# Performance work log

Hardware: AMD Instinct MI355X
Metric: run time of the kernel (lower is better)

## Reference

```python
import jax, jax.numpy as jnp
import numpy as np

B, S, HID = 2, 2048, 2048
H, DH = 16, 128
SCALE = 1.0 / np.sqrt(DH)


def setup_inputs() -> dict:
    key = jax.random.key(0)
    ks = jax.random.split(key, 5)
    std = 1.0 / np.sqrt(HID)
    return {
        "x": jax.random.normal(ks[0], (B, S, HID), dtype=jnp.float32),
        "wq": jax.random.normal(ks[1], (HID, HID), dtype=jnp.float32) * std,
        "wk": jax.random.normal(ks[2], (HID, HID), dtype=jnp.float32) * std,
        "wv": jax.random.normal(ks[3], (HID, HID), dtype=jnp.float32) * std,
        "wo": jax.random.normal(ks[4], (HID, HID), dtype=jnp.float32) * std,
    }


def reference(x, wq, wk, wv, wo):
    # nn.Linear(h, h, bias=False): y = x @ W^T
    q = (x @ wq.T).reshape(B, S, H, DH).transpose(0, 2, 1, 3)  # [B,H,S,Dh]
    k = (x @ wk.T).reshape(B, S, H, DH).transpose(0, 2, 1, 3)
    v = (x @ wv.T).reshape(B, S, H, DH).transpose(0, 2, 1, 3)
    scores = jnp.einsum("bhsd,bhtd->bhst", q, k) * SCALE  # [B,H,S,S]
    attn = jax.nn.softmax(scores.astype(jnp.float32), axis=-1).astype(q.dtype)
    # dropout p=0.0 (eval): identity
    out = jnp.einsum("bhst,bhtd->bhsd", attn, v)  # [B,H,S,Dh]
    out = out.transpose(0, 2, 1, 3).reshape(B, S, HID)
    return out @ wo.T
```

## Files before the change

kernel.cpp:

```cpp
#include <hip/hip_runtime.h>
#include <hip/hip_bf16.h>
#include <stdint.h>

typedef __attribute__((ext_vector_type(8))) short short8;
typedef __attribute__((ext_vector_type(4))) short short4v;
typedef __attribute__((ext_vector_type(4))) float f32x4;
typedef __attribute__((ext_vector_type(4))) unsigned int uint4v;

static __device__ __forceinline__ ushort f2bf(float f) {
    uint32_t u = __builtin_bit_cast(uint32_t, f);
    uint32_t r = (u + 0x7FFFu + ((u >> 16) & 1u)) >> 16;
    return (ushort)r;
}

static __device__ __forceinline__ uint32_t cvt_pk_bf16(float lo, float hi) {
    uint32_t d;
    asm("v_cvt_pk_bf16_f32 %0, %1, %2" : "=v"(d) : "v"(lo), "v"(hi));
    return d;
}

static __device__ __forceinline__ void async_copy16(const void* g, void* l) {
    __builtin_amdgcn_global_load_lds(
        (const __attribute__((address_space(1))) uint32_t*)g,
        (__attribute__((address_space(3))) uint32_t*)l, 16, 0, 0);
}

#define TR16(P3, IMM)                                                        \
    ({                                                                       \
        short4v _d;                                                          \
        asm volatile("ds_read_b64_tr_b16 %0, %1 offset:" #IMM                \
                     : "=v"(_d) : "v"(P3));                                  \
        _d;                                                                  \
    })

#define CAT8(a, b) __builtin_shufflevector(a, b, 0, 1, 2, 3, 4, 5, 6, 7)

__global__ __launch_bounds__(256) void cast_kernel(const float* __restrict__ in,
                                                   ushort* __restrict__ out, int n4) {
    int i = blockIdx.x * 256 + threadIdx.x;
    if (i >= n4) return;
    float4 v = reinterpret_cast<const float4*>(in)[i];
    uint2 o;
    o.x = cvt_pk_bf16(v.x, v.y);
    o.y = cvt_pk_bf16(v.z, v.w);
    reinterpret_cast<uint2*>(out)[i] = o;
}

__global__ __launch_bounds__(256) void cast3_kernel(const float* __restrict__ a,
                                                    const float* __restrict__ b,
                                                    const float* __restrict__ c,
                                                    ushort* __restrict__ out, int n4each) {
    int i = blockIdx.x * 256 + threadIdx.x;
    int which = i / n4each;
    int j = i - which * n4each;
    const float* src = which == 0 ? a : (which == 1 ? b : c);
    if (which > 2) return;
    float4 v = reinterpret_cast<const float4*>(src)[j];
    uint2 o;
    o.x = cvt_pk_bf16(v.x, v.y);
    o.y = cvt_pk_bf16(v.z, v.w);
    reinterpret_cast<uint2*>(out)[i] = o;
}

static __device__ __forceinline__ void store_val(float* C, size_t idx, float v) { C[idx] = v; }
static __device__ __forceinline__ void store_val(ushort* C, size_t idx, float v) { C[idx] = f2bf(v); }

template <typename OutT>
__global__ __launch_bounds__(256) void gemm_bt_kernel(const ushort* __restrict__ A,
                                                      const ushort* __restrict__ B,
                                                      OutT* __restrict__ C,
                                                      int M, int N, int K) {
    __shared__ __align__(16) ushort As[128 * 32];
    __shared__ __align__(16) ushort Bs[128 * 32];
    const int tid = threadIdx.x;
    const int w = tid >> 6, lane = tid & 63;
    const int fr = lane & 15, fq = lane >> 4;
    const int wr = w >> 1, wc = w & 1;
    const int bpn = N >> 7;
    const int which = blockIdx.x / bpn;
    const int row0 = blockIdx.y * 128;
    const int gcol0 = blockIdx.x * 128;
    const int col0 = gcol0 - which * N;
    OutT* Cw = C + (size_t)which * M * N;

    const int srow = tid >> 2;
    const int scol = (tid & 3) * 8;
    const ushort* ga0 = A + (size_t)(row0 + srow) * K + scol;
    const ushort* ga1 = A + (size_t)(row0 + 64 + srow) * K + scol;
    const ushort* gb0 = B + (size_t)(gcol0 + srow) * K + scol;
    const ushort* gb1 = B + (size_t)(gcol0 + 64 + srow) * K + scol;
    ushort* la0 = &As[(w * 64) * 8];
    ushort* la1 = &As[(256 + w * 64) * 8];
    ushort* lb0 = &Bs[(w * 64) * 8];
    ushort* lb1 = &Bs[(256 + w * 64) * 8];

    f32x4 acc[4][4];
#pragma unroll
    for (int m = 0; m < 4; ++m)
#pragma unroll
        for (int n = 0; n < 4; ++n) acc[m][n] = f32x4{0.f, 0.f, 0.f, 0.f};

    for (int kt = 0; kt < K; kt += 32) {
        __syncthreads();
        async_copy16(ga0 + kt, la0);
        async_copy16(ga1 + kt, la1);
        async_copy16(gb0 + kt, lb0);
        async_copy16(gb1 + kt, lb1);
        __syncthreads();
        short8 af[4], bfr[4];
#pragma unroll
        for (int m = 0; m < 4; ++m)
            af[m] = *(const short8*)&As[(wr * 64 + m * 16 + fr) * 32 + fq * 8];
#pragma unroll
        for (int n = 0; n < 4; ++n)
            bfr[n] = *(const short8*)&Bs[(wc * 64 + n * 16 + fr) * 32 + fq * 8];
#pragma unroll
        for (int m = 0; m < 4; ++m)
#pragma unroll
            for (int n = 0; n < 4; ++n)
                acc[m][n] = __builtin_amdgcn_mfma_f32_16x16x32_bf16(af[m], bfr[n], acc[m][n], 0, 0, 0);
    }

#pragma unroll
    for (int m = 0; m < 4; ++m) {
        const int grow = row0 + wr * 64 + m * 16 + fq * 4;
#pragma unroll
        for (int n = 0; n < 4; ++n) {
            const int gcol = col0 + wc * 64 + n * 16 + fr;
#pragma unroll
            for (int r = 0; r < 4; ++r)
                store_val(Cw, (size_t)(grow + r) * N + gcol, acc[m][n][r]);
        }
    }
}

__global__ __launch_bounds__(512, 2) void gemm256_kernel(const ushort* __restrict__ A,
                                                         const ushort* __restrict__ B,
                                                         ushort* __restrict__ C,
                                                         int M, int N, int K) {
    __shared__ __align__(16) char smem[131072];
    const int tid = threadIdx.x, w = tid >> 6, lane = tid & 63;
    const int fr = lane & 15, fq = lane >> 4;
    const int wm = w >> 2, wn = w & 3;
    const int bpn = N >> 8;
    const int which = blockIdx.x / bpn;
    const int row0 = blockIdx.y * 256;
    const int gcol0 = blockIdx.x * 256;
    const int col0 = gcol0 - which * N;
    ushort* Cw = C + (size_t)which * M * N;

    const int lo = ((tid & 7) ^ ((tid >> 3) & 7)) << 4;
    const int r0p = ((tid >> 3) << 1) + (lo >> 6);
    const int colE = (lo & 63) >> 1;
    const ushort* Ap0 = A + (size_t)(row0 + r0p) * K + colE;
    const ushort* Ap1 = A + (size_t)(row0 + 128 + r0p) * K + colE;
    const ushort* Bp0 = B + (size_t)(gcol0 + r0p) * K + colE;
    const ushort* Bp1 = B + (size_t)(gcol0 + 128 + r0p) * K + colE;

    char* aregs = smem;
    char* bregs = smem + 65536;
    const int wbyte = w * 1024;

    auto stageH = [&](int h) {
        const int kc = (h >> 1) * 64 + (h & 1) * 32;
        char* ar = aregs + (h & 3) * 16384;
        char* br = bregs + (h & 3) * 16384;
        async_copy16(Ap0 + kc, ar + wbyte);
        async_copy16(Ap1 + kc, ar + 8192 + wbyte);
        async_copy16(Bp0 + kc, br + wbyte);
        async_copy16(Bp1 + kc, br + 8192 + wbyte);
    };

    const int swz = ((fr & 1) * 64 + fq * 16) ^ (((fr >> 1) & 7) << 4);
    const int aBase = (wm * 64 + (fr >> 1)) * 128 + swz;
    const int bBase = (wn * 32 + (fr >> 1)) * 128 + swz;

    f32x4 acc[8][4];
#pragma unroll
    for (int m = 0; m < 8; ++m)
#pragma unroll
        for (int n = 0; n < 4; ++n) acc[m][n] = f32x4{0.f, 0.f, 0.f, 0.f};

    const int nH = K >> 5;
    stageH(0); stageH(1); stageH(2);
    asm volatile("s_waitcnt vmcnt(8)\n\ts_barrier" ::: "memory");

    for (int i = 0; i < nH; ++i) {
        if (i + 3 < nH) stageH(i + 3);
        const char* ar = aregs + (i & 3) * 16384 + aBase;
        const char* br = bregs + (i & 3) * 16384 + bBase;
        short8 af[8], bf[4];
#pragma unroll
        for (int m = 0; m < 8; ++m) af[m] = *(const short8*)(ar + m * 1024);
#pragma unroll
        for (int n = 0; n < 4; ++n) bf[n] = *(const short8*)(br + n * 1024);
        __builtin_amdgcn_s_setprio(1);
#pragma unroll
        for (int m = 0; m < 8; ++m)
#pragma unroll
            for (int n = 0; n < 4; ++n)
                acc[m][n] = __builtin_amdgcn_mfma_f32_16x16x32_bf16(af[m], bf[n], acc[m][n], 0, 0, 0);
        __builtin_amdgcn_s_setprio(0);
        if (i < nH - 3)
            asm volatile("s_waitcnt vmcnt(8)\n\ts_barrier" ::: "memory");
        else if (i == nH - 3)
            asm volatile("s_waitcnt vmcnt(4)\n\ts_barrier" ::: "memory");
        else if (i == nH - 2)
            asm volatile("s_waitcnt vmcnt(0)\n\ts_barrier" ::: "memory");
    }

#pragma unroll
    for (int m = 0; m < 8; ++m) {
        const int grow = row0 + wm * 128 + m * 16 + fq * 4;
#pragma unroll
        for (int n = 0; n < 4; ++n) {
            const int gcol = col0 + wn * 64 + n * 16 + fr;
#pragma unroll
            for (int r2 = 0; r2 < 4; ++r2)
                Cw[(size_t)(grow + r2) * N + gcol] = f2bf(acc[m][n][r2]);
        }
    }
}

__global__ __launch_bounds__(512) void attn_kernel(const ushort* __restrict__ Q,
                                                   const ushort* __restrict__ K,
                                                   const ushort* __restrict__ V,
                                                   ushort* __restrict__ O,
                                                   int S, int HID, float scale) {
    __shared__ __align__(16) ushort Ks[64 * 128];
    __shared__ __align__(16) ushort Vs[64 * 128];

    const int tid = threadIdx.x, w = tid >> 6, lane = tid & 63;
    const int fr = lane & 15, fq = lane >> 4;
    const int qt = blockIdx.x, h = blockIdx.y, b = blockIdx.z;
    const size_t rs = (size_t)HID;
    const int qr0 = qt * 128 + w * 16;
    const float c1 = scale * 1.4426950408889634f;

    short8 qf[4];
    {
        const ushort* qp = Q + ((size_t)(b * S) + qr0 + fr) * rs + h * 128 + fq * 8;
#pragma unroll
        for (int ks = 0; ks < 4; ++ks) qf[ks] = *(const short8*)(qp + ks * 32);
    }

    f32x4 of[8];
#pragma unroll
    for (int n = 0; n < 8; ++n) of[n] = f32x4{0.f, 0.f, 0.f, 0.f};
    float m2 = -1e30f;
    float l = 0.f;

    const ushort* Kb = K + (size_t)(b * S) * rs + h * 128;
    const ushort* Vb = V + (size_t)(b * S) * rs + h * 128;

    size_t koff[2];
#pragma unroll
    for (int j = 0; j < 2; ++j) {
        int row = j * 32 + w * 4 + (lane >> 4);
        int colb = ((lane & 15) * 16) ^ ((row & 7) << 4);
        koff[j] = (size_t)row * rs + (colb >> 1);
    }
    size_t voff[2];
#pragma unroll
    for (int j = 0; j < 2; ++j) {
        int L = j * 64 + w * 8 + (lane >> 3);
        int kv = (L >> 3) * 4 + ((lane >> 1) & 3);
        int dh = (L & 7) * 16 + (lane & 1) * 8;
        voff[j] = (size_t)kv * rs + dh;
    }

    const __attribute__((address_space(3))) ushort* vb3 =
        (const __attribute__((address_space(3))) ushort*)((const char*)Vs + fq * 2048 + fr * 8);

    const int srcA = fr + 16 * ((2 * fq) & 3);
    const int srcB = fr + 16 * ((2 * fq + 1) & 3);
    const int par = fq >> 1;

    const int nt = S / 64;
    for (int t = 0; t < nt; ++t) {
        __syncthreads();
        const ushort* kt0 = Kb + (size_t)t * 64 * rs;
        const ushort* vt0 = Vb + (size_t)t * 64 * rs;
#pragma unroll
        for (int j = 0; j < 2; ++j)
            async_copy16(kt0 + koff[j], &Ks[j * 4096 + w * 512]);
#pragma unroll
        for (int j = 0; j < 2; ++j)
            async_copy16(vt0 + voff[j], &Vs[j * 4096 + w * 512]);
        __syncthreads();

        f32x4 sf[4];
        __builtin_amdgcn_s_setprio(1);
#pragma unroll
        for (int kc = 0; kc < 4; ++kc) {
            f32x4 s = f32x4{0.f, 0.f, 0.f, 0.f};
#pragma unroll
            for (int ks = 0; ks < 4; ++ks) {
                int row = kc * 16 + fr;
                int pb = (row * 256 + ks * 64 + fq * 16) ^ ((row & 7) << 4);
                short8 kf = *(const short8*)((const char*)Ks + pb);
                s = __builtin_amdgcn_mfma_f32_16x16x32_bf16(kf, qf[ks], s, 0, 0, 0);
            }
            sf[kc] = s;
        }
        __builtin_amdgcn_s_setprio(0);

        float pm = fmaxf(fmaxf(fmaxf(sf[0][0], sf[0][1]), fmaxf(sf[0][2], sf[0][3])),
                         fmaxf(fmaxf(sf[1][0], sf[1][1]), fmaxf(sf[1][2], sf[1][3])));
        pm = fmaxf(pm, fmaxf(fmaxf(fmaxf(sf[2][0], sf[2][1]), fmaxf(sf[2][2], sf[2][3])),
                             fmaxf(fmaxf(sf[3][0], sf[3][1]), fmaxf(sf[3][2], sf[3][3]))));
        pm = fmaxf(pm, __shfl_xor(pm, 16));
        pm = fmaxf(pm, __shfl_xor(pm, 32));
        float pm2 = pm * c1;
        const bool noresc = __all(pm2 - m2 <= 8.0f);
        float sc = 1.0f;
        if (!noresc) {
            float m2new = fmaxf(m2, pm2);
            sc = exp2f(m2 - m2new);
            m2 = m2new;
        }
        float rsum = 0.f;
#pragma unroll
        for (int kc = 0; kc < 4; ++kc)
#pragma unroll
            for (int r = 0; r < 4; ++r) {
                float p = exp2f(sf[kc][r] * c1 - m2);
                sf[kc][r] = p;
                rsum += p;
            }
        rsum += __shfl_xor(rsum, 16);
        rsum += __shfl_xor(rsum, 32);
        if (noresc) {
            l = l + rsum;
        } else {
            l = l * sc + rsum;
#pragma unroll
            for (int n = 0; n < 8; ++n) {
                f32x4 o = of[n];
                o[0] *= sc; o[1] *= sc; o[2] *= sc; o[3] *= sc;
                of[n] = o;
            }
        }

        uint32_t cpk[4][2];
#pragma unroll
        for (int kc = 0; kc < 4; ++kc)
#pragma unroll
            for (int hh = 0; hh < 2; ++hh)
                cpk[kc][hh] = cvt_pk_bf16(sf[kc][2 * hh], sf[kc][2 * hh + 1]);

        __builtin_amdgcn_s_setprio(1);
        {
            uint32_t eA0 = __shfl(cpk[0][0], srcA), eA1 = __shfl(cpk[0][1], srcA);
            uint32_t oA0 = __shfl(cpk[1][0], srcA), oA1 = __shfl(cpk[1][1], srcA);
            uint32_t eB0 = __shfl(cpk[0][0], srcB), eB1 = __shfl(cpk[0][1], srcB);
            uint32_t oB0 = __shfl(cpk[1][0], srcB), oB1 = __shfl(cpk[1][1], srcB);
            uint4v pd;
            pd[0] = par ? oA0 : eA0; pd[1] = par ? oA1 : eA1;
            pd[2] = par ? oB0 : eB0; pd[3] = par ? oB1 : eB1;
            short8 pf = __builtin_bit_cast(short8, pd);
            {
                short4v a0 = TR16(vb3, 0),    b0 = TR16(vb3, 1024);
                short4v a1 = TR16(vb3, 128),  b1 = TR16(vb3, 1152);
                short4v a2 = TR16(vb3, 256),  b2 = TR16(vb3, 1280);
                short4v a3 = TR16(vb3, 384),  b3 = TR16(vb3, 1408);
                asm volatile("s_waitcnt lgkmcnt(0)" ::: "memory");
                __builtin_amdgcn_sched_barrier(0);
                of[0] = __builtin_amdgcn_mfma_f32_16x16x32_bf16(CAT8(a0, b0), pf, of[0], 0, 0, 0);
                of[1] = __builtin_amdgcn_mfma_f32_16x16x32_bf16(CAT8(a1, b1), pf, of[1], 0, 0, 0);
                of[2] = __builtin_amdgcn_mfma_f32_16x16x32_bf16(CAT8(a2, b2), pf, of[2], 0, 0, 0);
                of[3] = __builtin_amdgcn_mfma_f32_16x16x32_bf16(CAT8(a3, b3), pf, of[3], 0, 0, 0);
            }
            {
                short4v a0 = TR16(vb3, 512),  b0 = TR16(vb3, 1536);
                short4v a1 = TR16(vb3, 640),  b1 = TR16(vb3, 1664);
                short4v a2 = TR16(vb3, 768),  b2 = TR16(vb3, 1792);
                short4v a3 = TR16(vb3, 896),  b3 = TR16(vb3, 1920);
                asm volatile("s_waitcnt lgkmcnt(0)" ::: "memory");
                __builtin_amdgcn_sched_barrier(0);
                of[4] = __builtin_amdgcn_mfma_f32_16x16x32_bf16(CAT8(a0, b0), pf, of[4], 0, 0, 0);
                of[5] = __builtin_amdgcn_mfma_f32_16x16x32_bf16(CAT8(a1, b1), pf, of[5], 0, 0, 0);
                of[6] = __builtin_amdgcn_mfma_f32_16x16x32_bf16(CAT8(a2, b2), pf, of[6], 0, 0, 0);
                of[7] = __builtin_amdgcn_mfma_f32_16x16x32_bf16(CAT8(a3, b3), pf, of[7], 0, 0, 0);
            }
        }
        {
            uint32_t eA0 = __shfl(cpk[2][0], srcA), eA1 = __shfl(cpk[2][1], srcA);
            uint32_t oA0 = __shfl(cpk[3][0], srcA), oA1 = __shfl(cpk[3][1], srcA);
            uint32_t eB0 = __shfl(cpk[2][0], srcB), eB1 = __shfl(cpk[2][1], srcB);
            uint32_t oB0 = __shfl(cpk[3][0], srcB), oB1 = __shfl(cpk[3][1], srcB);
            uint4v pd;
            pd[0] = par ? oA0 : eA0; pd[1] = par ? oA1 : eA1;
            pd[2] = par ? oB0 : eB0; pd[3] = par ? oB1 : eB1;
            short8 pf = __builtin_bit_cast(short8, pd);
            {
                short4v a0 = TR16(vb3, 8192), b0 = TR16(vb3, 9216);
                short4v a1 = TR16(vb3, 8320), b1 = TR16(vb3, 9344);
                short4v a2 = TR16(vb3, 8448), b2 = TR16(vb3, 9472);
                short4v a3 = TR16(vb3, 8576), b3 = TR16(vb3, 9600);
                asm volatile("s_waitcnt lgkmcnt(0)" ::: "memory");
                __builtin_amdgcn_sched_barrier(0);
                of[0] = __builtin_amdgcn_mfma_f32_16x16x32_bf16(CAT8(a0, b0), pf, of[0], 0, 0, 0);
                of[1] = __builtin_amdgcn_mfma_f32_16x16x32_bf16(CAT8(a1, b1), pf, of[1], 0, 0, 0);
                of[2] = __builtin_amdgcn_mfma_f32_16x16x32_bf16(CAT8(a2, b2), pf, of[2], 0, 0, 0);
                of[3] = __builtin_amdgcn_mfma_f32_16x16x32_bf16(CAT8(a3, b3), pf, of[3], 0, 0, 0);
            }
            {
                short4v a0 = TR16(vb3, 8704), b0 = TR16(vb3, 9728);
                short4v a1 = TR16(vb3, 8832), b1 = TR16(vb3, 9856);
                short4v a2 = TR16(vb3, 8960), b2 = TR16(vb3, 9984);
                short4v a3 = TR16(vb3, 9088), b3 = TR16(vb3, 10112);
                asm volatile("s_waitcnt lgkmcnt(0)" ::: "memory");
                __builtin_amdgcn_sched_barrier(0);
                of[4] = __builtin_amdgcn_mfma_f32_16x16x32_bf16(CAT8(a0, b0), pf, of[4], 0, 0, 0);
                of[5] = __builtin_amdgcn_mfma_f32_16x16x32_bf16(CAT8(a1, b1), pf, of[5], 0, 0, 0);
                of[6] = __builtin_amdgcn_mfma_f32_16x16x32_bf16(CAT8(a2, b2), pf, of[6], 0, 0, 0);
                of[7] = __builtin_amdgcn_mfma_f32_16x16x32_bf16(CAT8(a3, b3), pf, of[7], 0, 0, 0);
            }
        }
        __builtin_amdgcn_s_setprio(0);
    }

    float inv = 1.f / l;
    ushort* ob = O + ((size_t)(b * S) + qr0 + fr) * rs + h * 128 + fq * 4;
#pragma unroll
    for (int n = 0; n < 8; ++n) {
        uint2 o2;
        o2.x = cvt_pk_bf16(of[n][0] * inv, of[n][1] * inv);
        o2.y = cvt_pk_bf16(of[n][2] * inv, of[n][3] * inv);
        *reinterpret_cast<uint2*>(ob + n * 16) = o2;
    }
}

extern "C" void kernel_launch(void* const* d_in, const int* in_sizes, int n_in,
                              void* d_out, int out_size, void* d_ws, size_t ws_size,
                              hipStream_t stream) {
    constexpr int B = 2, S = 2048, HID = 2048, H = 16;
    constexpr int M = B * S;
    const float scale = 0.08838834764831845f;

    const float* x  = (const float*)d_in[0];
    const float* wq = (const float*)d_in[1];
    const float* wk = (const float*)d_in[2];
    const float* wv = (const float*)d_in[3];
    const float* wo = (const float*)d_in[4];
    float* out = (float*)d_out;

    char* ws = (char*)d_ws;
    ushort* xb  = (ushort*)(ws);
    ushort* wqb = (ushort*)(ws + 16777216);
    ushort* qb  = (ushort*)(ws + 41943040);
    ushort* kb  = (ushort*)(ws + 58720256);
    ushort* vb  = (ushort*)(ws + 75497472);

    const int XN = M * HID;
    const int WN = HID * HID;

    cast_kernel<<<XN / 4 / 256, 256, 0, stream>>>(x, xb, XN / 4);
    cast3_kernel<<<3 * WN / 4 / 256, 256, 0, stream>>>(wq, wk, wv, wqb, WN / 4);

    dim3 gq(3 * HID / 256, M / 256);
    gemm256_kernel<<<gq, 512, 0, stream>>>(xb, wqb, qb, M, HID, HID);

    dim3 ga(S / 128, H, B);
    attn_kernel<<<ga, 512, 0, stream>>>(qb, kb, vb, xb, S, HID, scale);

    cast_kernel<<<WN / 4 / 256, 256, 0, stream>>>(wo, wqb, WN / 4);
    dim3 gg(HID / 128, M / 128);
    gemm_bt_kernel<float><<<gg, 256, 0, stream>>>(xb, wqb, out, M, HID, HID);
}
```

Measured before the change: 326.1 us.

## Compute V transposed via separate GEMM and read V^T directly in attention

Result: no change. 322.7 us (-1.0%).

```diff
diff --git a/kernel.cpp b/kernel.cpp
--- a/kernel.cpp
+++ b/kernel.cpp
@@ -3,7 +3,6 @@
 #include <stdint.h>
 
 typedef __attribute__((ext_vector_type(8))) short short8;
-typedef __attribute__((ext_vector_type(4))) short short4v;
 typedef __attribute__((ext_vector_type(4))) float f32x4;
 typedef __attribute__((ext_vector_type(4))) unsigned int uint4v;
 
@@ -24,16 +23,6 @@
         (const __attribute__((address_space(1))) uint32_t*)g,
         (__attribute__((address_space(3))) uint32_t*)l, 16, 0, 0);
 }
-
-#define TR16(P3, IMM)                                                        \
-    ({                                                                       \
-        short4v _d;                                                          \
-        asm volatile("ds_read_b64_tr_b16 %0, %1 offset:" #IMM                \
-                     : "=v"(_d) : "v"(P3));                                  \
-        _d;                                                                  \
-    })
-
-#define CAT8(a, b) __builtin_shufflevector(a, b, 0, 1, 2, 3, 4, 5, 6, 7)
 
 __global__ __launch_bounds__(256) void cast_kernel(const float* __restrict__ in,
                                                    ushort* __restrict__ out, int n4) {
@@ -224,16 +213,17 @@
 
 __global__ __launch_bounds__(512) void attn_kernel(const ushort* __restrict__ Q,
                                                    const ushort* __restrict__ K,
-                                                   const ushort* __restrict__ V,
+                                                   const ushort* __restrict__ VT,
                                                    ushort* __restrict__ O,
                                                    int S, int HID, float scale) {
     __shared__ __align__(16) ushort Ks[64 * 128];
-    __shared__ __align__(16) ushort Vs[64 * 128];
+    __shared__ __align__(16) ushort Vts[128 * 64];
 
     const int tid = threadIdx.x, w = tid >> 6, lane = tid & 63;
     const int fr = lane & 15, fq = lane >> 4;
-    const int qt = blockIdx.x, h = blockIdx.y, b = blockIdx.z;
+    const int h = blockIdx.x & 15, b = blockIdx.x >> 4, qt = blockIdx.y;
     const size_t rs = (size_t)HID;
+    const size_t vs = (size_t)(2 * S);
     const int qr0 = qt * 128 + w * 16;
     const float c1 = scale * 1.4426950408889634f;
 
@@ -251,7 +241,7 @@
     float l = 0.f;
 
     const ushort* Kb = K + (size_t)(b * S) * rs + h * 128;
-    const ushort* Vb = V + (size_t)(b * S) * rs + h * 128;
+    const ushort* Vb = VT + (size_t)(h * 128) * vs + b * S;
 
     size_t koff[2];
 #pragma unroll
@@ -260,17 +250,13 @@
         int colb = ((lane & 15) * 16) ^ ((row & 7) << 4);
         koff[j] = (size_t)row * rs + (colb >> 1);
     }
-    size_t voff[2];
+    size_t vtoff[2];
 #pragma unroll
     for (int j = 0; j < 2; ++j) {
-        int L = j * 64 + w * 8 + (lane >> 3);
-        int kv = (L >> 3) * 4 + ((lane >> 1) & 3);
-        int dh = (L & 7) * 16 + (lane & 1) * 8;
-        voff[j] = (size_t)kv * rs + dh;
-    }
-
-    const __attribute__((address_space(3))) ushort* vb3 =
-        (const __attribute__((address_space(3))) ushort*)((const char*)Vs + fq * 2048 + fr * 8);
+        int row = j * 64 + (tid >> 3);
+        int colb = ((tid & 7) * 16) ^ ((row & 7) << 4);
+        vtoff[j] = (size_t)row * vs + (colb >> 1);
+    }
 
     const int srcA = fr + 16 * ((2 * fq) & 3);
     const int srcB = fr + 16 * ((2 * fq + 1) & 3);
@@ -280,13 +266,13 @@
     for (int t = 0; t < nt; ++t) {
         __syncthreads();
         const ushort* kt0 = Kb + (size_t)t * 64 * rs;
-        const ushort* vt0 = Vb + (size_t)t * 64 * rs;
+        const ushort* vt0 = Vb + (size_t)t * 64;
 #pragma unroll
         for (int j = 0; j < 2; ++j)
             async_copy16(kt0 + koff[j], &Ks[j * 4096 + w * 512]);
 #pragma unroll
         for (int j = 0; j < 2; ++j)
-            async_copy16(vt0 + voff[j], &Vs[j * 4096 + w * 512]);
+            async_copy16(vt0 + vtoff[j], &Vts[j * 4096 + w * 512]);
         __syncthreads();
 
         f32x4 sf[4];
@@ -350,72 +336,22 @@
                 cpk[kc][hh] = cvt_pk_bf16(sf[kc][2 * hh], sf[kc][2 * hh + 1]);
 
         __builtin_amdgcn_s_setprio(1);
-        {
-            uint32_t eA0 = __shfl(cpk[0][0], srcA), eA1 = __shfl(cpk[0][1], srcA);
-            uint32_t oA0 = __shfl(cpk[1][0], srcA), oA1 = __shfl(cpk[1][1], srcA);
-            uint32_t eB0 = __shfl(cpk[0][0], srcB), eB1 = __shfl(cpk[0][1], srcB);
-            uint32_t oB0 = __shfl(cpk[1][0], srcB), oB1 = __shfl(cpk[1][1], srcB);
+#pragma unroll
+        for (int kvc = 0; kvc < 2; ++kvc) {
+            uint32_t eA0 = __shfl(cpk[2 * kvc][0], srcA), eA1 = __shfl(cpk[2 * kvc][1], srcA);
+            uint32_t oA0 = __shfl(cpk[2 * kvc + 1][0], srcA), oA1 = __shfl(cpk[2 * kvc + 1][1], srcA);
+            uint32_t eB0 = __shfl(cpk[2 * kvc][0], srcB), eB1 = __shfl(cpk[2 * kvc][1], srcB);
+            uint32_t oB0 = __shfl(cpk[2 * kvc + 1][0], srcB), oB1 = __shfl(cpk[2 * kvc + 1][1], srcB);
             uint4v pd;
             pd[0] = par ? oA0 : eA0; pd[1] = par ? oA1 : eA1;
             pd[2] = par ? oB0 : eB0; pd[3] = par ? oB1 : eB1;
             short8 pf = __builtin_bit_cast(short8, pd);
-            {
-                short4v a0 = TR16(vb3, 0),    b0 = TR16(vb3, 1024);
-                short4v a1 = TR16(vb3, 128),  b1 = TR16(vb3, 1152);
-                short4v a2 = TR16(vb3, 256),  b2 = TR16(vb3, 1280);
-                short4v a3 = TR16(vb3, 384),  b3 = TR16(vb3, 1408);
-                asm volatile("s_waitcnt lgkmcnt(0)" ::: "memory");
-                __builtin_amdgcn_sched_barrier(0);
-                of[0] = __builtin_amdgcn_mfma_f32_16x16x32_bf16(CAT8(a0, b0), pf, of[0], 0, 0, 0);
-                of[1] = __builtin_amdgcn_mfma_f32_16x16x32_bf16(CAT8(a1, b1), pf, of[1], 0, 0, 0);
-                of[2] = __builtin_amdgcn_mfma_f32_16x16x32_bf16(CAT8(a2, b2), pf, of[2], 0, 0, 0);
-                of[3] = __builtin_amdgcn_mfma_f32_16x16x32_bf16(CAT8(a3, b3), pf, of[3], 0, 0, 0);
-            }
-            {
-                short4v a0 = TR16(vb3, 512),  b0 = TR16(vb3, 1536);
-                short4v a1 = TR16(vb3, 640),  b1 = TR16(vb3, 1664);
-                short4v a2 = TR16(vb3, 768),  b2 = TR16(vb3, 1792);
-                short4v a3 = TR16(vb3, 896),  b3 = TR16(vb3, 1920);
-                asm volatile("s_waitcnt lgkmcnt(0)" ::: "memory");
-                __builtin_amdgcn_sched_barrier(0);
-                of[4] = __builtin_amdgcn_mfma_f32_16x16x32_bf16(CAT8(a0, b0), pf, of[4], 0, 0, 0);
-                of[5] = __builtin_amdgcn_mfma_f32_16x16x32_bf16(CAT8(a1, b1), pf, of[5], 0, 0, 0);
-                of[6] = __builtin_amdgcn_mfma_f32_16x16x32_bf16(CAT8(a2, b2), pf, of[6], 0, 0, 0);
-                of[7] = __builtin_amdgcn_mfma_f32_16x16x32_bf16(CAT8(a3, b3), pf, of[7], 0, 0, 0);
-            }
-        }
-        {
-            uint32_t eA0 = __shfl(cpk[2][0], srcA), eA1 = __shfl(cpk[2][1], srcA);
-            uint32_t oA0 = __shfl(cpk[3][0], srcA), oA1 = __shfl(cpk[3][1], srcA);
-            uint32_t eB0 = __shfl(cpk[2][0], srcB), eB1 = __shfl(cpk[2][1], srcB);
-            uint32_t oB0 = __shfl(cpk[3][0], srcB), oB1 = __shfl(cpk[3][1], srcB);
-            uint4v pd;
-            pd[0] = par ? oA0 : eA0; pd[1] = par ? oA1 : eA1;
-            pd[2] = par ? oB0 : eB0; pd[3] = par ? oB1 : eB1;
-            short8 pf = __builtin_bit_cast(short8, pd);
-            {
-                short4v a0 = TR16(vb3, 8192), b0 = TR16(vb3, 9216);
-                short4v a1 = TR16(vb3, 8320), b1 = TR16(vb3, 9344);
-                short4v a2 = TR16(vb3, 8448), b2 = TR16(vb3, 9472);
-                short4v a3 = TR16(vb3, 8576), b3 = TR16(vb3, 9600);
-                asm volatile("s_waitcnt lgkmcnt(0)" ::: "memory");
-                __builtin_amdgcn_sched_barrier(0);
-                of[0] = __builtin_amdgcn_mfma_f32_16x16x32_bf16(CAT8(a0, b0), pf, of[0], 0, 0, 0);
-                of[1] = __builtin_amdgcn_mfma_f32_16x16x32_bf16(CAT8(a1, b1), pf, of[1], 0, 0, 0);
-                of[2] = __builtin_amdgcn_mfma_f32_16x16x32_bf16(CAT8(a2, b2), pf, of[2], 0, 0, 0);
-                of[3] = __builtin_amdgcn_mfma_f32_16x16x32_bf16(CAT8(a3, b3), pf, of[3], 0, 0, 0);
-            }
-            {
-                short4v a0 = TR16(vb3, 8704), b0 = TR16(vb3, 9728);
-                short4v a1 = TR16(vb3, 8832), b1 = TR16(vb3, 9856);
-                short4v a2 = TR16(vb3, 8960), b2 = TR16(vb3, 9984);
-                short4v a3 = TR16(vb3, 9088), b3 = TR16(vb3, 10112);
-                asm volatile("s_waitcnt lgkmcnt(0)" ::: "memory");
-                __builtin_amdgcn_sched_barrier(0);
-                of[4] = __builtin_amdgcn_mfma_f32_16x16x32_bf16(CAT8(a0, b0), pf, of[4], 0, 0, 0);
-                of[5] = __builtin_amdgcn_mfma_f32_16x16x32_bf16(CAT8(a1, b1), pf, of[5], 0, 0, 0);
-                of[6] = __builtin_amdgcn_mfma_f32_16x16x32_bf16(CAT8(a2, b2), pf, of[6], 0, 0, 0);
-                of[7] = __builtin_amdgcn_mfma_f32_16x16x32_bf16(CAT8(a3, b3), pf, of[7], 0, 0, 0);
+#pragma unroll
+            for (int n = 0; n < 8; ++n) {
+                int row = n * 16 + fr;
+                int pb = row * 128 + ((kvc * 64 + fq * 16) ^ ((row & 7) << 4));
+                short8 vf = *(const short8*)((const char*)Vts + pb);
+                of[n] = __builtin_amdgcn_mfma_f32_16x16x32_bf16(vf, pf, of[n], 0, 0, 0);
             }
         }
         __builtin_amdgcn_s_setprio(0);
@@ -449,9 +385,10 @@
     char* ws = (char*)d_ws;
     ushort* xb  = (ushort*)(ws);
     ushort* wqb = (ushort*)(ws + 16777216);
+    ushort* wvb = (ushort*)(ws + 33554432);
     ushort* qb  = (ushort*)(ws + 41943040);
     ushort* kb  = (ushort*)(ws + 58720256);
-    ushort* vb  = (ushort*)(ws + 75497472);
+    ushort* vtb = (ushort*)(ws + 75497472);
 
     const int XN = M * HID;
     const int WN = HID * HID;
@@ -459,11 +396,14 @@
     cast_kernel<<<XN / 4 / 256, 256, 0, stream>>>(x, xb, XN / 4);
     cast3_kernel<<<3 * WN / 4 / 256, 256, 0, stream>>>(wq, wk, wv, wqb, WN / 4);
 
-    dim3 gq(3 * HID / 256, M / 256);
+    dim3 gq(2 * HID / 256, M / 256);
     gemm256_kernel<<<gq, 512, 0, stream>>>(xb, wqb, qb, M, HID, HID);
 
-    dim3 ga(S / 128, H, B);
-    attn_kernel<<<ga, 512, 0, stream>>>(qb, kb, vb, xb, S, HID, scale);
+    dim3 gv(M / 128, HID / 128);
+    gemm_bt_kernel<ushort><<<gv, 256, 0, stream>>>(wvb, xb, vtb, HID, M, HID);
+
+    dim3 ga(H * B, S / 128);
+    attn_kernel<<<ga, 512, 0, stream>>>(qb, kb, vtb, xb, S, HID, scale);
 
     cast_kernel<<<WN / 4 / 256, 256, 0, stream>>>(wo, wqb, WN / 4);
     dim3 gg(HID / 128, M / 128);
```
